# Kernel optimization log

Hardware: AMD Instinct MI355X
Metric: run time of the kernel (lower is better)

Reference implementation:

```python
import jax, jax.numpy as jnp
import numpy as np

B, CIN, HW = 32, 64, 56
K, KS, STRIDE, PAD = 128, 3, 1, 1


def setup_inputs() -> dict:
    key = jax.random.key(0)
    kx, kw, kb = jax.random.split(key, 3)
    x = jax.random.normal(kx, (B, CIN, HW, HW), dtype=jnp.float32)
    weight = jax.random.normal(kw, (K, CIN, KS, KS), dtype=jnp.float32)
    offset = jax.random.normal(kb, (K, 1, 1), dtype=jnp.float32)
    return {"x": x, "weight": weight, "offset": offset}


def reference(x, weight, offset):
    # conv2d (NCHW, OIHW) with stride/padding, then add per-kernel scalar offset.
    # Equivalent to the module's im2col (create_window_column_matrix) + matmul
    # + reshape, plus self.offset broadcast over (B, K, s, s).
    out = jax.lax.conv_general_dilated(
        x, weight,
        window_strides=(STRIDE, STRIDE),
        padding=[(PAD, PAD), (PAD, PAD)],
        dimension_numbers=("NCHW", "OIHW", "NCHW"),
    )
    return out + offset  # offset (K,1,1) broadcasts against (B,K,s,s)
```

## Files before the change

kernel.cpp:

```cpp
#include <hip/hip_runtime.h>
#include <hip/hip_bf16.h>

namespace {

using frag_t    = __attribute__((ext_vector_type(8))) short;
using f32x4     = __attribute__((ext_vector_type(4))) float;
using float4_t  = __attribute__((ext_vector_type(4))) float;

constexpr int BATCH = 32;
constexpr int CIN   = 64;
constexpr int HWD   = 56;
constexpr int KOUT  = 128;
constexpr int SP    = HWD * HWD;
constexpr int KD    = 9 * CIN;
constexpr int BN    = 128;
constexpr int HALO  = 57;
constexpr int NEXT  = BN + 2 * HALO;
constexpr int NTILES= SP / BN + 1;
constexpr int TT    = BATCH * (SP / 64);
constexpr int WB    = (KOUT * KD + 255) / 256;

__device__ inline unsigned short f2bf(float f) {
    __hip_bfloat16 h = __float2bfloat16(f);
    return __builtin_bit_cast(unsigned short, h);
}

__global__ __launch_bounds__(256)
void prep_kernel(const float* __restrict__ x, const float* __restrict__ w,
                 unsigned short* __restrict__ wpA, unsigned short* __restrict__ xT)
{
    if (blockIdx.x >= TT) {
        const int idx = (blockIdx.x - TT) * 256 + threadIdx.x;
        if (idx < KOUT * KD) {
            const int kout = idx / KD, kk = idx - kout * KD;
            const int kc = kk >> 5, e = kk & 31;
            const int t = kk >> 6, c = kk & 63;
            const int ky = t / 3, kx = t - ky * 3;
            wpA[(kc * KOUT + kout) * 32 + e] = f2bf(w[((kout * CIN + c) * 3 + ky) * 3 + kx]);
        }
        return;
    }
    __shared__ float ls[64][68];
    const int bb   = blockIdx.x / (SP / 64);
    const int tile = blockIdx.x - bb * (SP / 64);
    const int sp0  = tile * 64;
    const int tid  = threadIdx.x;
    const int cq   = tid >> 4;
    const int spo  = (tid & 15) * 4;
    const float* xb = x + (size_t)bb * CIN * SP;
    #pragma unroll
    for (int j = 0; j < 4; ++j) {
        const int c = cq + 16 * j;
        float4_t v = *(const float4_t*)&xb[(size_t)c * SP + sp0 + spo];
        ls[spo + 0][c] = v.x; ls[spo + 1][c] = v.y;
        ls[spo + 2][c] = v.z; ls[spo + 3][c] = v.w;
    }
    __syncthreads();
    unsigned short* xo = xT + (size_t)(bb * SP + sp0) * 64;
    #pragma unroll
    for (int j = 0; j < 2; ++j) {
        const int s  = tid + 256 * j;
        const int sp = s >> 3, e = s & 7;
        frag_t u;
        #pragma unroll
        for (int q = 0; q < 8; ++q)
            u[q] = (short)f2bf(ls[sp][e * 8 + q]);
        *(frag_t*)&xo[sp * 64 + e * 8] = u;
    }
}

__global__ __launch_bounds__(256, 2)
void conv_mfma(const unsigned short* __restrict__ xT, const unsigned short* __restrict__ wpA,
               const float* __restrict__ off, float* __restrict__ out)
{
    __shared__ unsigned short xs[NEXT * 64];

    const int b    = blockIdx.y;
    const int sp0  = blockIdx.x * BN;
    const int tid  = threadIdx.x;
    const int lane = tid & 63;
    const int wid  = tid >> 6;

    {
        const unsigned short* xb = xT + (size_t)b * SP * 64;
        #pragma unroll
        for (int it = 0; it < 8; ++it) {
            const int s = it * 256 + tid;
            if (s < NEXT * 8) {
                const int r = s >> 3, e = s & 7;
                int g = sp0 - HALO + r;
                g = min(max(g, 0), SP - 1);
                frag_t v = *(const frag_t*)&xb[(size_t)g * 64 + e * 8];
                *(frag_t*)&xs[r * 64 + ((e * 8) ^ ((r & 7) << 3))] = v;
            }
        }
    }
    __syncthreads();

    const int wm  = (wid >> 1) * 64;
    const int wn  = (wid & 1) * 64;
    const int l15 = lane & 15;
    const int l4  = lane >> 4;

    unsigned long long mbits = 0ull;
    #pragma unroll
    for (int t = 0; t < 9; ++t) {
        const int dy = t / 3 - 1, dx = t % 3 - 1;
        #pragma unroll
        for (int nf = 0; nf < 4; ++nf) {
            const int sp = sp0 + wn + nf * 16 + l15;
            const int y  = sp / HWD;
            const int xc = sp - y * HWD;
            const bool v = ((unsigned)(y + dy) < (unsigned)HWD) &
                           ((unsigned)(xc + dx) < (unsigned)HWD);
            mbits |= (unsigned long long)(v ? 1 : 0) << (t * 4 + nf);
        }
    }

    const unsigned short* abase = wpA + (wm + l15) * 32 + 8 * l4;

    f32x4 acc[4][4] = {};
    const frag_t zf = {0,0,0,0,0,0,0,0};
    const int cread = 8 * l4;

    #pragma unroll
    for (int kc = 0; kc < 18; ++kc) {
        const int t  = kc >> 1;
        const int c0 = (kc & 1) * 32;
        const int s    = (t / 3 - 1) * HWD + (t % 3 - 1);
        const int row0 = wn + l15 + HALO + s;
        const int sw   = (row0 & 7) << 3;
        frag_t a[4], bfr[4];
        #pragma unroll
        for (int mi = 0; mi < 4; ++mi)
            a[mi] = *(const frag_t*)(abase + kc * (KOUT * 32) + mi * (16 * 32));
        #pragma unroll
        for (int nf = 0; nf < 4; ++nf) {
            const frag_t bl = *(const frag_t*)&xs[(row0 + 16 * nf) * 64
                                                 + ((c0 + cread) ^ sw)];
            const bool v = (mbits >> (t * 4 + nf)) & 1;
            bfr[nf] = v ? bl : zf;
        }
        #pragma unroll
        for (int mi = 0; mi < 4; ++mi)
            #pragma unroll
            for (int nf = 0; nf < 4; ++nf)
                acc[mi][nf] = __builtin_amdgcn_mfma_f32_16x16x32_bf16(
                    a[mi], bfr[nf], acc[mi][nf], 0, 0, 0);
    }

    const int spn = sp0 + wn + l15;
    #pragma unroll
    for (int mi = 0; mi < 4; ++mi) {
        const int km = wm + 16 * mi + 4 * l4;
        #pragma unroll
        for (int reg = 0; reg < 4; ++reg) {
            const int  kk  = km + reg;
            const float ofv = off[kk];
            float* ob = out + (size_t)(b * KOUT + kk) * SP;
            #pragma unroll
            for (int nf = 0; nf < 4; ++nf) {
                const int sp = spn + 16 * nf;
                if (sp < SP) ob[sp] = acc[mi][nf][reg] + ofv;
            }
        }
    }
}

__global__ __launch_bounds__(256)
void conv3x3_kernel(const float* __restrict__ x, const float* __restrict__ w,
                    const float* __restrict__ off, float* __restrict__ out)
{
    const int s  = blockIdx.x * 256 + threadIdx.x;
    const int b  = s / SP;
    const int sp = s - b * SP;
    const int y  = sp / HWD;
    const int xx = sp - y * HWD;
    const int k0 = blockIdx.y * 4;

    const int   xm1 = (xx > 0) ? xx - 1 : 0;
    const int   xp1 = (xx < HWD - 1) ? xx + 1 : HWD - 1;
    const float m0  = (xx > 0) ? 1.f : 0.f;
    const float m2  = (xx < HWD - 1) ? 1.f : 0.f;

    int ro[3]; float msk[3][3];
    #pragma unroll
    for (int ky = 0; ky < 3; ++ky) {
        const int  yy = y + ky - 1;
        const bool ok = (unsigned)yy < (unsigned)HWD;
        const float rm = ok ? 1.f : 0.f;
        ro[ky] = (ok ? yy : 0) * HWD;
        msk[ky][0] = rm * m0; msk[ky][1] = rm; msk[ky][2] = rm * m2;
    }
    float acc[4] = {0.f, 0.f, 0.f, 0.f};
    const float* xb = x + (size_t)b * CIN * SP;
    for (int c = 0; c < CIN; ++c) {
        const float* xc = xb + (size_t)c * SP;
        #pragma unroll
        for (int ky = 0; ky < 3; ++ky) {
            const float* xr = xc + ro[ky];
            const float v0 = xr[xm1] * msk[ky][0];
            const float v1 = xr[xx]  * msk[ky][1];
            const float v2 = xr[xp1] * msk[ky][2];
            const int wi = c * 9 + ky * 3;
            #pragma unroll
            for (int kk = 0; kk < 4; ++kk) {
                const float* wr = w + (size_t)(k0 + kk) * (CIN * 9) + wi;
                acc[kk] = fmaf(v0, wr[0], acc[kk]);
                acc[kk] = fmaf(v1, wr[1], acc[kk]);
                acc[kk] = fmaf(v2, wr[2], acc[kk]);
            }
        }
    }
    #pragma unroll
    for (int kk = 0; kk < 4; ++kk)
        out[(size_t)(b * KOUT + k0 + kk) * SP + sp] = acc[kk] + off[k0 + kk];
}

}

extern "C" void kernel_launch(void* const* d_in, const int* in_sizes, int n_in,
                              void* d_out, int out_size, void* d_ws, size_t ws_size,
                              hipStream_t stream)
{
    const float* x   = (const float*)d_in[0];
    const float* w   = (const float*)d_in[1];
    const float* off = (const float*)d_in[2];
    float* out = (float*)d_out;

    const size_t wpa_bytes = (size_t)KOUT * KD * 2;
    const size_t xt_bytes  = (size_t)BATCH * SP * CIN * 2;

    if (ws_size >= wpa_bytes + xt_bytes) {
        unsigned short* wpA = (unsigned short*)d_ws;
        unsigned short* xT  = (unsigned short*)((char*)d_ws + wpa_bytes);
        prep_kernel<<<TT + WB, 256, 0, stream>>>(x, w, wpA, xT);
        dim3 grid(NTILES, BATCH);
        conv_mfma<<<grid, dim3(256, 1, 1), 0, stream>>>(xT, wpA, off, out);
    } else {
        dim3 grid((BATCH * SP) / 256, KOUT / 4);
        conv3x3_kernel<<<grid, dim3(256, 1, 1), 0, stream>>>(x, w, off, out);
    }
}
```

Before: 45.16 us.

## Make conv kernel persistent with double-buffered direct-to-LDS tile loads

Replaces the one-tile-per-block grid with a fixed grid of 512 blocks that each process up to two tiles. The second tile's input is loaded straight into a second LDS buffer via global_load_lds while the first tile computes, and the tile order is remapped across blocks. The aim is to hide input staging latency behind MFMA work and cut the block count. In exchange it doubles LDS per block, which can lower occupancy, and leaves the work unevenly spread because only some blocks get a second tile.

```diff
diff --git a/kernel.cpp b/kernel.cpp
--- a/kernel.cpp
+++ b/kernel.cpp
@@ -17,6 +17,8 @@
 constexpr int HALO  = 57;
 constexpr int NEXT  = BN + 2 * HALO;
 constexpr int NTILES= SP / BN + 1;
+constexpr int NTT   = NTILES * BATCH;
+constexpr int NBLK  = 512;
 constexpr int TT    = BATCH * (SP / 64);
 constexpr int WB    = (KOUT * KD + 255) / 256;
 
@@ -70,100 +72,131 @@
 }
 
 __global__ __launch_bounds__(256, 2)
-void conv_mfma(const unsigned short* __restrict__ xT, const unsigned short* __restrict__ wpA,
+void conv_pipe(const unsigned short* __restrict__ xT, const unsigned short* __restrict__ wpA,
                const float* __restrict__ off, float* __restrict__ out)
 {
-    __shared__ unsigned short xs[NEXT * 64];
-
-    const int b    = blockIdx.y;
-    const int sp0  = blockIdx.x * BN;
+    __shared__ unsigned short xs[2][NEXT * 64];
+
+    const int bid  = blockIdx.x;
+    const int wk0  = (bid & 7) * (NBLK / 8) + (bid >> 3);
     const int tid  = threadIdx.x;
     const int lane = tid & 63;
     const int wid  = tid >> 6;
-
-    {
+    const int lsw  = ((lane & 7) * 8) ^ ((lane >> 3) << 3);
+
+    const int wm   = (wid >> 1) * 64;
+    const int wn   = (wid & 1) * 64;
+    const int l15  = lane & 15;
+    const int l4   = lane >> 4;
+    const unsigned short* abase = wpA + (size_t)(wm + l15) * 32 + 8 * l4;
+    const int cread = 8 * l4;
+
+    auto stage = [&](int buf, int tile) {
+        const int b   = tile / NTILES;
+        const int sp0 = (tile - b * NTILES) * BN;
         const unsigned short* xb = xT + (size_t)b * SP * 64;
         #pragma unroll
         for (int it = 0; it < 8; ++it) {
-            const int s = it * 256 + tid;
-            if (s < NEXT * 8) {
-                const int r = s >> 3, e = s & 7;
+            const int R0 = it * 32 + wid * 8;
+            const int r  = R0 + (lane >> 3);
+            if (r < NEXT) {
                 int g = sp0 - HALO + r;
                 g = min(max(g, 0), SP - 1);
-                frag_t v = *(const frag_t*)&xb[(size_t)g * 64 + e * 8];
-                *(frag_t*)&xs[r * 64 + ((e * 8) ^ ((r & 7) << 3))] = v;
-            }
-        }
-    }
-    __syncthreads();
-
-    const int wm  = (wid >> 1) * 64;
-    const int wn  = (wid & 1) * 64;
-    const int l15 = lane & 15;
-    const int l4  = lane >> 4;
-
-    unsigned long long mbits = 0ull;
-    #pragma unroll
-    for (int t = 0; t < 9; ++t) {
-        const int dy = t / 3 - 1, dx = t % 3 - 1;
+                __builtin_amdgcn_global_load_lds(
+                    (const __attribute__((address_space(1))) unsigned int*)
+                        (xb + (size_t)g * 64 + lsw),
+                    (__attribute__((address_space(3))) unsigned int*)
+                        &xs[buf][R0 * 64 + lane * 8],
+                    16, 0, 0);
+            }
+        }
+    };
+
+    auto compute = [&](int buf, int tile) {
+        const int b   = tile / NTILES;
+        const int sp0 = (tile - b * NTILES) * BN;
+
+        unsigned long long mbits = 0ull;
+        int yv[4], xv[4];
         #pragma unroll
         for (int nf = 0; nf < 4; ++nf) {
             const int sp = sp0 + wn + nf * 16 + l15;
-            const int y  = sp / HWD;
-            const int xc = sp - y * HWD;
-            const bool v = ((unsigned)(y + dy) < (unsigned)HWD) &
-                           ((unsigned)(xc + dx) < (unsigned)HWD);
-            mbits |= (unsigned long long)(v ? 1 : 0) << (t * 4 + nf);
-        }
-    }
-
-    const unsigned short* abase = wpA + (wm + l15) * 32 + 8 * l4;
-
-    f32x4 acc[4][4] = {};
-    const frag_t zf = {0,0,0,0,0,0,0,0};
-    const int cread = 8 * l4;
-
-    #pragma unroll
-    for (int kc = 0; kc < 18; ++kc) {
-        const int t  = kc >> 1;
-        const int c0 = (kc & 1) * 32;
-        const int s    = (t / 3 - 1) * HWD + (t % 3 - 1);
-        const int row0 = wn + l15 + HALO + s;
-        const int sw   = (row0 & 7) << 3;
-        frag_t a[4], bfr[4];
-        #pragma unroll
-        for (int mi = 0; mi < 4; ++mi)
-            a[mi] = *(const frag_t*)(abase + kc * (KOUT * 32) + mi * (16 * 32));
-        #pragma unroll
-        for (int nf = 0; nf < 4; ++nf) {
-            const frag_t bl = *(const frag_t*)&xs[(row0 + 16 * nf) * 64
-                                                 + ((c0 + cread) ^ sw)];
-            const bool v = (mbits >> (t * 4 + nf)) & 1;
-            bfr[nf] = v ? bl : zf;
-        }
-        #pragma unroll
-        for (int mi = 0; mi < 4; ++mi)
-            #pragma unroll
-            for (int nf = 0; nf < 4; ++nf)
-                acc[mi][nf] = __builtin_amdgcn_mfma_f32_16x16x32_bf16(
-                    a[mi], bfr[nf], acc[mi][nf], 0, 0, 0);
-    }
-
-    const int spn = sp0 + wn + l15;
-    #pragma unroll
-    for (int mi = 0; mi < 4; ++mi) {
-        const int km = wm + 16 * mi + 4 * l4;
-        #pragma unroll
-        for (int reg = 0; reg < 4; ++reg) {
-            const int  kk  = km + reg;
-            const float ofv = off[kk];
-            float* ob = out + (size_t)(b * KOUT + kk) * SP;
+            yv[nf] = sp / HWD;
+            xv[nf] = sp - yv[nf] * HWD;
+        }
+        #pragma unroll
+        for (int t = 0; t < 9; ++t) {
+            const int dy = t / 3 - 1, dx = t % 3 - 1;
             #pragma unroll
             for (int nf = 0; nf < 4; ++nf) {
-                const int sp = spn + 16 * nf;
-                if (sp < SP) ob[sp] = acc[mi][nf][reg] + ofv;
-            }
-        }
+                const bool v = ((unsigned)(yv[nf] + dy) < (unsigned)HWD) &
+                               ((unsigned)(xv[nf] + dx) < (unsigned)HWD);
+                mbits |= (unsigned long long)(v ? 1 : 0) << (t * 4 + nf);
+            }
+        }
+
+        const frag_t zf = {0,0,0,0,0,0,0,0};
+        f32x4 acc[4][4] = {};
+        const unsigned short* xsb = &xs[buf][0];
+
+        #pragma unroll
+        for (int kc = 0; kc < 18; ++kc) {
+            const int t  = kc >> 1;
+            const int c0 = (kc & 1) * 32;
+            const int s    = (t / 3 - 1) * HWD + (t % 3 - 1);
+            const int row0 = wn + l15 + HALO + s;
+            const int sw   = (row0 & 7) << 3;
+            frag_t a[4], bfr[4];
+            #pragma unroll
+            for (int mi = 0; mi < 4; ++mi)
+                a[mi] = *(const frag_t*)(abase + (size_t)(kc * KOUT + mi * 16) * 32);
+            #pragma unroll
+            for (int nf = 0; nf < 4; ++nf) {
+                const frag_t bl = *(const frag_t*)&xsb[(row0 + 16 * nf) * 64
+                                                      + ((c0 + cread) ^ sw)];
+                bfr[nf] = ((mbits >> (t * 4 + nf)) & 1) ? bl : zf;
+            }
+            #pragma unroll
+            for (int mi = 0; mi < 4; ++mi)
+                #pragma unroll
+                for (int nf = 0; nf < 4; ++nf)
+                    acc[mi][nf] = __builtin_amdgcn_mfma_f32_16x16x32_bf16(
+                        a[mi], bfr[nf], acc[mi][nf], 0, 0, 0);
+        }
+
+        const int spn = sp0 + wn + l15;
+        #pragma unroll
+        for (int mi = 0; mi < 4; ++mi) {
+            const int km = wm + 16 * mi + 4 * l4;
+            #pragma unroll
+            for (int reg = 0; reg < 4; ++reg) {
+                const int  kk  = km + reg;
+                const float ofv = off[kk];
+                float* ob = out + (size_t)(b * KOUT + kk) * SP;
+                #pragma unroll
+                for (int nf = 0; nf < 4; ++nf) {
+                    const int sp = spn + 16 * nf;
+                    if (sp < SP) ob[sp] = acc[mi][nf][reg] + ofv;
+                }
+            }
+        }
+    };
+
+    const int t0 = wk0;
+    const int t1 = wk0 + NBLK;
+    const bool has2 = (t1 < NTT);
+
+    stage(0, t0);
+    asm volatile("s_waitcnt vmcnt(0)" ::: "memory");
+    __syncthreads();
+
+    if (has2) stage(1, t1);
+    compute(0, t0);
+
+    if (has2) {
+        asm volatile("s_waitcnt vmcnt(0)" ::: "memory");
+        __syncthreads();
+        compute(1, t1);
     }
 }
 
@@ -235,8 +268,7 @@
         unsigned short* wpA = (unsigned short*)d_ws;
         unsigned short* xT  = (unsigned short*)((char*)d_ws + wpa_bytes);
         prep_kernel<<<TT + WB, 256, 0, stream>>>(x, w, wpA, xT);
-        dim3 grid(NTILES, BATCH);
-        conv_mfma<<<grid, dim3(256, 1, 1), 0, stream>>>(xT, wpA, off, out);
+        conv_pipe<<<NBLK, dim3(256, 1, 1), 0, stream>>>(xT, wpA, off, out);
     } else {
         dim3 grid((BATCH * SP) / 256, KOUT / 4);
         conv3x3_kernel<<<grid, dim3(256, 1, 1), 0, stream>>>(x, w, off, out);
```

Result: slower. 52.29 us (+15.8%).
